# Optimization experiments

Hardware: AMD Instinct MI355X
Metric: run time of the kernel (lower is better)

Reference implementation:

```python
import jax, jax.numpy as jnp
import numpy as np

D_MODEL = 1024
D_INNER = 1024
N_HEADS = 16
HEAD_DIM = D_INNER // N_HEADS  # 64
D_STATE = 16
DT_RANK = 16
CHUNK = 64
PROJ = 2 * D_INNER + 2 * D_STATE * N_HEADS + DT_RANK  # 2576


def setup_inputs() -> dict:
    key = jax.random.key(0)
    ks = jax.random.split(key, 6)
    B, S = 4, 4096
    x = jax.random.normal(ks[0], (B, S, D_MODEL), jnp.float32)
    W_in = jax.random.normal(ks[1], (PROJ, D_MODEL), jnp.float32) * 0.02
    dt_W = jax.random.normal(ks[2], (N_HEADS, DT_RANK), jnp.float32) * 0.1
    dt_b = jax.random.normal(ks[3], (N_HEADS,), jnp.float32) * 0.1
    A_log = jnp.full((N_HEADS,), jnp.log(0.5), jnp.float32)
    D_param = jnp.ones((N_HEADS,), jnp.float32)
    W_out = jax.random.normal(ks[4], (D_MODEL, D_INNER), jnp.float32) * 0.02
    norm_w = jnp.ones((D_INNER,), jnp.float32)
    return dict(x=x, W_in=W_in, dt_W=dt_W, dt_b=dt_b, A_log=A_log,
                D_param=D_param, W_out=W_out, norm_w=norm_w)


def _forward(x, W_in, dt_W, dt_b, A_log, D_param, W_out, norm_w):
    B, S, _ = x.shape
    H, P, N, K = N_HEADS, HEAD_DIM, D_STATE, CHUNK
    proj = x @ W_in.T  # (B,S,PROJ)
    xp = proj[..., :D_INNER]
    z = proj[..., D_INNER:2 * D_INNER]
    o = 2 * D_INNER
    B_ssm = proj[..., o:o + N * H].reshape(B, S, H, N)
    C_ssm = proj[..., o + N * H:o + 2 * N * H].reshape(B, S, H, N)
    dt_low = proj[..., o + 2 * N * H:]
    dt = jax.nn.softplus(dt_low @ dt_W.T + dt_b)  # (B,S,H)
    xp = xp.reshape(B, S, H, P)
    A = -jnp.exp(A_log)  # (H,)

    # --- chunked selective scan (SSD) ---
    nC = S // K  # S chosen divisible by K (original pads otherwise)
    xc = xp.reshape(B, nC, K, H, P)
    dtc = dt.reshape(B, nC, K, H)
    Bc = B_ssm.reshape(B, nC, K, H, N)
    Cc = C_ssm.reshape(B, nC, K, H, N)
    dA = dtc * A  # (B,nC,K,H)
    dAcs = jnp.cumsum(dA, axis=2)
    # intra-chunk quadratic (attention-like) form
    Lm = jnp.exp(dAcs[:, :, :, None, :] - dAcs[:, :, None, :, :])
    causal = jnp.tril(jnp.ones((K, K), jnp.float32))
    Lm = Lm * causal[None, None, :, :, None]
    scores = jnp.einsum('bcihn,bcjhn->bcijh', Cc, Bc) * Lm * dtc[:, :, None, :, :]
    y_intra = jnp.einsum('bcijh,bcjhp->bcihp', scores, xc)
    # per-chunk state contribution
    decay_to_end = jnp.exp(dAcs[:, :, -1:, :] - dAcs)
    wx = (dtc * decay_to_end)[..., None] * xc  # (B,nC,K,H,P)
    chunk_state = jnp.einsum('bckhn,bckhp->bchnp', Bc, wx)  # (B,nC,H,N,P)
    chunk_decay = jnp.exp(dAcs[:, :, -1, :])  # (B,nC,H)

    # cross-chunk recurrence: emit state at chunk START (matches torch loop)
    def step(h, inp):
        d, s = inp
        return d[:, :, None, None] * h + s, h
    h0 = jnp.zeros((B, H, N, P), jnp.float32)
    _, h_states = jax.lax.scan(
        step, h0,
        (jnp.moveaxis(chunk_decay, 1, 0), jnp.moveaxis(chunk_state, 1, 0)))
    h_states = jnp.moveaxis(h_states, 0, 1)  # (B,nC,H,N,P)

    y_cross = jnp.einsum('bcthn,bchnp,bcth->bcthp', Cc, h_states, jnp.exp(dAcs))
    y = (y_intra + y_cross).reshape(B, S, H, P)
    # --- end scan ---

    y = y + xp * D_param[None, None, :, None]
    y = y.reshape(B, S, D_INNER)
    rms = jnp.sqrt(jnp.mean(y * y, axis=-1, keepdims=True) + 1e-6)
    y = y / rms * norm_w
    y = y * jax.nn.silu(z)
    return y @ W_out.T


def reference(x, W_in, dt_W, dt_b, A_log, D_param, W_out, norm_w):
    return _forward(x, W_in, dt_W, dt_b, A_log, D_param, W_out, norm_w)
```

## Files before the change

kernel.cpp:

```cpp
#include <hip/hip_runtime.h>

typedef unsigned short u16;
typedef __attribute__((ext_vector_type(8))) short short8;
typedef __attribute__((ext_vector_type(4))) float f32x4;
typedef __attribute__((ext_vector_type(4))) unsigned short u16x4;
typedef __attribute__((ext_vector_type(8))) unsigned short u16x8;

#define BTOK 16384
#define PROJ_N 2576
#define PROJ_PAD 2688
#define DK 1024
#define NCH 256
#define NH 16
#define HD 64
#define NS 16

__device__ __forceinline__ float b2f(u16 b) {
    union { unsigned int u; float f; } v; v.u = ((unsigned int)b) << 16; return v.f;
}
__device__ __forceinline__ u16 f2b(float f) {
    union { float f; unsigned int u; } v; v.f = f;
    unsigned int r = v.u + 0x7fffu + ((v.u >> 16) & 1u);
    return (u16)(r >> 16);
}
__device__ __forceinline__ void gl_lds16(const u16* g, u16* l) {
    __builtin_amdgcn_global_load_lds((__attribute__((address_space(1))) void*)g,
                                     (__attribute__((address_space(3))) void*)l,
                                     16, 0, 0);
}

__global__ __launch_bounds__(256) void cast_bf16(const float* __restrict__ s,
                                                 u16* __restrict__ d, int n4) {
    int t = blockIdx.x * 256 + threadIdx.x;
    if (t < n4) {
        float4 v = ((const float4*)s)[t];
        u16x4 o; o.x = f2b(v.x); o.y = f2b(v.y); o.z = f2b(v.z); o.w = f2b(v.w);
        ((u16x4*)d)[t] = o;
    }
}

__global__ __launch_bounds__(256) void cast_pad_win(const float* __restrict__ s,
                                                    u16* __restrict__ d) {
    int t = blockIdx.x * 256 + threadIdx.x;
    int i4 = t * 4;
    float4 v = make_float4(0.f, 0.f, 0.f, 0.f);
    if (i4 < PROJ_N * DK) v = ((const float4*)s)[t];
    u16x4 o; o.x = f2b(v.x); o.y = f2b(v.y); o.z = f2b(v.z); o.w = f2b(v.w);
    ((u16x4*)d)[t] = o;
}

template <int OUT_BF16>
__global__ __launch_bounds__(256) void gemm_bt(const u16* __restrict__ A,
                                               const u16* __restrict__ B,
                                               float* __restrict__ Cf,
                                               u16* __restrict__ Cb,
                                               int K, int ldc) {
    __shared__ u16 As[128 * 64];
    __shared__ u16 Bs[128 * 64];
    const int tid = threadIdx.x;
    const int bm = blockIdx.x, bn = blockIdx.y;
    const int wave = tid >> 6, lane = tid & 63;
    const int wm = (wave >> 1) * 64, wn = (wave & 1) * 64;
    const int m_l = lane & 15, quad = lane >> 4;

    f32x4 acc[4][4];
#pragma unroll
    for (int i = 0; i < 4; ++i)
#pragma unroll
        for (int j = 0; j < 4; ++j) acc[i][j] = (f32x4){0.f, 0.f, 0.f, 0.f};

    const u16* Ab = A + (long)bm * 128 * K;
    const u16* Bb = B + (long)bn * 128 * K;

    for (int k0 = 0; k0 < K; k0 += 64) {
#pragma unroll
        for (int it = 0; it < 4; ++it) {
            int li = it * 256 + tid;
            int r = li >> 3;
            int k8 = (li & 7) ^ (r & 7);
            u16* lbase = &As[(it * 256 + wave * 64) * 8];
            gl_lds16(Ab + (long)r * K + k0 + k8 * 8, lbase);
            u16* lbaseB = &Bs[(it * 256 + wave * 64) * 8];
            gl_lds16(Bb + (long)r * K + k0 + k8 * 8, lbaseB);
        }
        __syncthreads();
#pragma unroll
        for (int ks = 0; ks < 2; ++ks) {
            const int k8 = ks * 4 + quad;
            const int slot = k8 ^ (m_l & 7);
            short8 af[4], bf[4];
#pragma unroll
            for (int i = 0; i < 4; ++i) af[i] = *(const short8*)(&As[(wm + i * 16 + m_l) * 64 + slot * 8]);
#pragma unroll
            for (int j = 0; j < 4; ++j) bf[j] = *(const short8*)(&Bs[(wn + j * 16 + m_l) * 64 + slot * 8]);
#pragma unroll
            for (int i = 0; i < 4; ++i)
#pragma unroll
                for (int j = 0; j < 4; ++j)
                    acc[i][j] = __builtin_amdgcn_mfma_f32_16x16x32_bf16(af[i], bf[j], acc[i][j], 0, 0, 0);
        }
        __syncthreads();
    }
#pragma unroll
    for (int i = 0; i < 4; ++i) {
        int row_base = bm * 128 + wm + i * 16 + quad * 4;
#pragma unroll
        for (int j = 0; j < 4; ++j) {
            int col = bn * 128 + wn + j * 16 + m_l;
#pragma unroll
            for (int r = 0; r < 4; ++r) {
                float v = acc[i][j][r];
                long off = (long)(row_base + r) * ldc + col;
                if (OUT_BF16) Cb[off] = f2b(v);
                else          Cf[off] = v;
            }
        }
    }
}

__global__ __launch_bounds__(64) void compute_dt(const u16* __restrict__ proj,
                                                 const float* __restrict__ dt_W,
                                                 const float* __restrict__ dt_b,
                                                 const float* __restrict__ A_log,
                                                 float* __restrict__ dt,
                                                 float* __restrict__ dAcs,
                                                 float* __restrict__ decay) {
    int bc = blockIdx.x;
    int i = threadIdx.x;
    long tok = (long)bc * 64 + i;
    float low[16];
#pragma unroll
    for (int r = 0; r < 16; ++r) low[r] = b2f(proj[tok * PROJ_PAD + 2560 + r]);
#pragma unroll
    for (int h = 0; h < 16; ++h) {
        float a = dt_b[h];
#pragma unroll
        for (int r = 0; r < 16; ++r) a += low[r] * dt_W[h * 16 + r];
        float d = (a > 20.f) ? a : log1pf(__expf(a));
        float dA = -__expf(A_log[h]) * d;
        float cs = dA;
#pragma unroll
        for (int off = 1; off < 64; off <<= 1) {
            float o = __shfl_up(cs, off, 64);
            if (i >= off) cs += o;
        }
        dt[tok * 16 + h] = d;
        dAcs[tok * 16 + h] = cs;
        if (i == 63) decay[bc * 16 + h] = __expf(cs);
    }
}

__global__ __launch_bounds__(256) void ssm_intra(const u16* __restrict__ proj,
                                                 const float* __restrict__ dt,
                                                 const float* __restrict__ dAcs,
                                                 u16* __restrict__ y_acc,
                                                 float* __restrict__ cstate) {
    int bch = blockIdx.x;
    int bc = bch >> 4, h = bch & 15;
    long tok0 = (long)bc * 64;
    __shared__ float Cs[64][16], Bm[64][16];
    __shared__ u16 Sh[64][64], Sl[64][64];
    __shared__ u16 Xt[64][64];
    __shared__ u16 Wh[64][64], Wl[64][64];
    __shared__ u16 Bt[16][64];
    __shared__ float dts[64], dAs[64], wk[64];
    const int tid = threadIdx.x;
    const int wave = tid >> 6, lane = tid & 63;
    const int m_l = lane & 15, quad = lane >> 4;

    if (tid < 64) {
        dts[tid] = dt[(tok0 + tid) * 16 + h];
        dAs[tid] = dAcs[(tok0 + tid) * 16 + h];
    }
    if (tid < 64) wk[tid] = dts[tid] * __expf(dAs[63] - dAs[tid]);
#pragma unroll
    for (int it = 0; it < 4; ++it) {
        int li = it * 256 + tid;
        int i = li >> 4, n = li & 15;
        u16 cb = proj[(tok0 + i) * PROJ_PAD + 2304 + h * 16 + n];
        u16 bb = proj[(tok0 + i) * PROJ_PAD + 2048 + h * 16 + n];
        Cs[i][n] = b2f(cb);
        Bm[i][n] = b2f(bb);
        Bt[n][i] = bb;
    }
    __syncthreads();
#pragma unroll
    for (int it = 0; it < 2; ++it) {
        int li = it * 256 + tid;
        int j = li & 63, p0 = (li >> 6) * 8;
        u16x8 xv = *(const u16x8*)&proj[(tok0 + j) * PROJ_PAD + h * 64 + p0];
        float w = wk[j];
#pragma unroll
        for (int t = 0; t < 8; ++t) {
            u16 xb = xv[t];
            Xt[p0 + t][j] = xb;
            float v = w * b2f(xb);
            u16 hi = f2b(v);
            Wh[p0 + t][j] = hi;
            Wl[p0 + t][j] = f2b(v - b2f(hi));
        }
    }
    {
        int j = tid & 63, i0 = tid >> 6;
#pragma unroll
        for (int g = 0; g < 16; ++g) {
            int i = i0 + g * 4;
            float v = 0.f;
            if (j <= i) {
                float d = 0.f;
                const f32x4* cp = (const f32x4*)Cs[i];
                const f32x4* bp = (const f32x4*)Bm[j];
#pragma unroll
                for (int n4 = 0; n4 < 4; ++n4) {
                    f32x4 c = cp[n4], b = bp[n4];
                    d += c.x * b.x + c.y * b.y + c.z * b.z + c.w * b.w;
                }
                v = d * __expf(dAs[i] - dAs[j]) * dts[j];
            }
            u16 hi = f2b(v);
            Sh[i][j] = hi;
            Sl[i][j] = f2b(v - b2f(hi));
        }
    }
    __syncthreads();
    {
        f32x4 yv[4];
#pragma unroll
        for (int jt = 0; jt < 4; ++jt) yv[jt] = (f32x4){0.f, 0.f, 0.f, 0.f};
#pragma unroll
        for (int ks = 0; ks < 2; ++ks) {
            int kc = ks * 32 + quad * 8;
            short8 ah = *(const short8*)&Sh[wave * 16 + m_l][kc];
            short8 al = *(const short8*)&Sl[wave * 16 + m_l][kc];
#pragma unroll
            for (int jt = 0; jt < 4; ++jt) {
                short8 bx = *(const short8*)&Xt[jt * 16 + m_l][kc];
                yv[jt] = __builtin_amdgcn_mfma_f32_16x16x32_bf16(ah, bx, yv[jt], 0, 0, 0);
                yv[jt] = __builtin_amdgcn_mfma_f32_16x16x32_bf16(al, bx, yv[jt], 0, 0, 0);
            }
        }
#pragma unroll
        for (int jt = 0; jt < 4; ++jt)
#pragma unroll
            for (int r = 0; r < 4; ++r) {
                int i = wave * 16 + quad * 4 + r;
                int p = jt * 16 + m_l;
                y_acc[(tok0 + i) * 1024 + h * 64 + p] = f2b(yv[jt][r]);
            }
    }
    {
        f32x4 cacc = (f32x4){0.f, 0.f, 0.f, 0.f};
#pragma unroll
        for (int ks = 0; ks < 2; ++ks) {
            int kc = ks * 32 + quad * 8;
            short8 a = *(const short8*)&Bt[m_l][kc];
            short8 bh = *(const short8*)&Wh[wave * 16 + m_l][kc];
            short8 bl = *(const short8*)&Wl[wave * 16 + m_l][kc];
            cacc = __builtin_amdgcn_mfma_f32_16x16x32_bf16(a, bh, cacc, 0, 0, 0);
            cacc = __builtin_amdgcn_mfma_f32_16x16x32_bf16(a, bl, cacc, 0, 0, 0);
        }
#pragma unroll
        for (int r = 0; r < 4; ++r) {
            int n = quad * 4 + r;
            int p = wave * 16 + m_l;
            cstate[(long)bch * 1024 + n * 64 + p] = cacc[r];
        }
    }
}

__global__ __launch_bounds__(256) void scan_chunks(const float* __restrict__ cs,
                                                   const float* __restrict__ decay,
                                                   float* __restrict__ hs) {
    int t = blockIdx.x * 256 + threadIdx.x;
    int p = t & 63, n = (t >> 6) & 15, h = (t >> 10) & 15, b = t >> 14;
    float state = 0.f;
    for (int c = 0; c < 64; ++c) {
        long idx = (((long)((b * 64 + c) * 16 + h)) * 16 + n) * 64 + p;
        hs[idx] = state;
        state = decay[(b * 64 + c) * 16 + h] * state + cs[idx];
    }
}

__global__ __launch_bounds__(256) void ssm_cross(const u16* __restrict__ proj,
                                                 const float* __restrict__ dAcs,
                                                 const float* __restrict__ hs,
                                                 const u16* __restrict__ y_acc,
                                                 const float* __restrict__ D_param,
                                                 u16* __restrict__ y_pre) {
    int bch = blockIdx.x;
    int bc = bch >> 4, h = bch & 15;
    long tok0 = (long)bc * 64;
    __shared__ float hss[16][64], Cs[64][16], dAs[64];
    int tid = threadIdx.x;
#pragma unroll
    for (int it = 0; it < 4; ++it) {
        int li = it * 256 + tid;
        hss[li >> 6][li & 63] = hs[(long)bch * 1024 + li];
        int i = li >> 4, n = li & 15;
        Cs[i][n] = b2f(proj[(tok0 + i) * PROJ_PAD + 2304 + h * 16 + n]);
    }
    if (tid < 64) dAs[tid] = dAcs[(tok0 + tid) * 16 + h];
    __syncthreads();
    float Dh = D_param[h];
    int pi = (tid & 15) * 4;
    int ib = tid >> 4;
#pragma unroll
    for (int g = 0; g < 4; ++g) {
        int i = ib + 16 * g;
        f32x4 cr = (f32x4){0.f, 0.f, 0.f, 0.f};
#pragma unroll
        for (int n = 0; n < 16; ++n) {
            float c = Cs[i][n];
            cr += c * *(const f32x4*)&hss[n][pi];
        }
        float e = __expf(dAs[i]);
        long off = (tok0 + i) * 1024 + h * 64 + pi;
        u16x4 ya = *(const u16x4*)&y_acc[off];
        u16x4 xv = *(const u16x4*)&proj[(tok0 + i) * PROJ_PAD + h * 64 + pi];
        u16x4 o;
        o.x = f2b(b2f(ya.x) + e * cr.x + b2f(xv.x) * Dh);
        o.y = f2b(b2f(ya.y) + e * cr.y + b2f(xv.y) * Dh);
        o.z = f2b(b2f(ya.z) + e * cr.z + b2f(xv.z) * Dh);
        o.w = f2b(b2f(ya.w) + e * cr.w + b2f(xv.w) * Dh);
        *(u16x4*)&y_pre[off] = o;
    }
}

__global__ __launch_bounds__(256) void norm_gate(const u16* __restrict__ proj,
                                                 const float* __restrict__ norm_w,
                                                 u16* __restrict__ y) {
    long tok = blockIdx.x;
    int tid = threadIdx.x;
    int c0 = tid * 4;
    u16x4 yv = *(const u16x4*)&y[tok * 1024 + c0];
    float v0 = b2f(yv.x), v1 = b2f(yv.y), v2 = b2f(yv.z), v3 = b2f(yv.w);
    float ss = v0 * v0 + v1 * v1 + v2 * v2 + v3 * v3;
    int lane = tid & 63, w = tid >> 6;
#pragma unroll
    for (int d = 32; d > 0; d >>= 1) ss += __shfl_down(ss, d, 64);
    __shared__ float red[4];
    if (lane == 0) red[w] = ss;
    __syncthreads();
    float tot = red[0] + red[1] + red[2] + red[3];
    float inv = rsqrtf(tot * (1.f / 1024.f) + 1e-6f);
    float4 nw = *(const float4*)&norm_w[c0];
    u16x4 zv = *(const u16x4*)&proj[tok * PROJ_PAD + 1024 + c0];
    float z0 = b2f(zv.x), z1 = b2f(zv.y), z2 = b2f(zv.z), z3 = b2f(zv.w);
    u16x4 o;
    o.x = f2b(v0 * inv * nw.x * (z0 / (1.f + __expf(-z0))));
    o.y = f2b(v1 * inv * nw.y * (z1 / (1.f + __expf(-z1))));
    o.z = f2b(v2 * inv * nw.z * (z2 / (1.f + __expf(-z2))));
    o.w = f2b(v3 * inv * nw.w * (z3 / (1.f + __expf(-z3))));
    *(u16x4*)&y[tok * 1024 + c0] = o;
}

extern "C" void kernel_launch(void* const* d_in, const int* in_sizes, int n_in,
                              void* d_out, int out_size, void* d_ws, size_t ws_size,
                              hipStream_t stream) {
    const float* x      = (const float*)d_in[0];
    const float* W_in   = (const float*)d_in[1];
    const float* dt_W   = (const float*)d_in[2];
    const float* dt_b   = (const float*)d_in[3];
    const float* A_log  = (const float*)d_in[4];
    const float* D_par  = (const float*)d_in[5];
    const float* W_out  = (const float*)d_in[6];
    const float* norm_w = (const float*)d_in[7];
    float* out = (float*)d_out;

    char* ws = (char*)d_ws;
    size_t off = 0;
    auto alloc = [&](size_t b) { void* p = ws + off; off += (b + 255) & ~(size_t)255; return p; };
    u16*   x_bf    = (u16*)alloc((size_t)BTOK * DK * 2);
    u16*   win_bf  = (u16*)alloc((size_t)PROJ_PAD * DK * 2);
    u16*   wout_bf = (u16*)alloc((size_t)DK * DK * 2);
    u16*   proj    = (u16*)alloc((size_t)BTOK * PROJ_PAD * 2);
    float* dt      = (float*)alloc((size_t)BTOK * NH * 4);
    float* dAcs    = (float*)alloc((size_t)BTOK * NH * 4);
    float* decay   = (float*)alloc((size_t)NCH * NH * 4);
    float* cstate  = (float*)alloc((size_t)NCH * NH * NS * HD * 4);
    float* hstates = (float*)alloc((size_t)NCH * NH * NS * HD * 4);
    u16*   y_pre   = (u16*)alloc((size_t)BTOK * DK * 2);
    u16*   y_acc   = x_bf;

    cast_bf16<<<BTOK * DK / 4 / 256, 256, 0, stream>>>(x, x_bf, BTOK * DK / 4);
    cast_bf16<<<DK * DK / 4 / 256, 256, 0, stream>>>(W_out, wout_bf, DK * DK / 4);
    cast_pad_win<<<PROJ_PAD * DK / 4 / 256, 256, 0, stream>>>(W_in, win_bf);

    gemm_bt<1><<<dim3(128, 21), 256, 0, stream>>>(x_bf, win_bf, nullptr, proj, DK, PROJ_PAD);

    compute_dt<<<NCH, 64, 0, stream>>>(proj, dt_W, dt_b, A_log, dt, dAcs, decay);
    ssm_intra<<<NCH * NH, 256, 0, stream>>>(proj, dt, dAcs, y_acc, cstate);
    scan_chunks<<<256, 256, 0, stream>>>(cstate, decay, hstates);
    ssm_cross<<<NCH * NH, 256, 0, stream>>>(proj, dAcs, hstates, y_acc, D_par, y_pre);
    norm_gate<<<BTOK, 256, 0, stream>>>(proj, norm_w, y_pre);

    gemm_bt<0><<<dim3(128, 8), 256, 0, stream>>>(y_pre, wout_bf, out, nullptr, DK, DK);
}
```

Measured before the change: 412.5 us.

## Fuse dt computation into ssm_intra and pad shared arrays against bank conflicts

```diff
diff --git a/kernel.cpp b/kernel.cpp
--- a/kernel.cpp
+++ b/kernel.cpp
@@ -118,61 +118,51 @@
     }
 }
 
-__global__ __launch_bounds__(64) void compute_dt(const u16* __restrict__ proj,
+__global__ __launch_bounds__(256) void ssm_intra(const u16* __restrict__ proj,
                                                  const float* __restrict__ dt_W,
                                                  const float* __restrict__ dt_b,
                                                  const float* __restrict__ A_log,
-                                                 float* __restrict__ dt,
                                                  float* __restrict__ dAcs,
-                                                 float* __restrict__ decay) {
-    int bc = blockIdx.x;
-    int i = threadIdx.x;
-    long tok = (long)bc * 64 + i;
-    float low[16];
-#pragma unroll
-    for (int r = 0; r < 16; ++r) low[r] = b2f(proj[tok * PROJ_PAD + 2560 + r]);
-#pragma unroll
-    for (int h = 0; h < 16; ++h) {
-        float a = dt_b[h];
-#pragma unroll
-        for (int r = 0; r < 16; ++r) a += low[r] * dt_W[h * 16 + r];
-        float d = (a > 20.f) ? a : log1pf(__expf(a));
-        float dA = -__expf(A_log[h]) * d;
-        float cs = dA;
-#pragma unroll
-        for (int off = 1; off < 64; off <<= 1) {
-            float o = __shfl_up(cs, off, 64);
-            if (i >= off) cs += o;
-        }
-        dt[tok * 16 + h] = d;
-        dAcs[tok * 16 + h] = cs;
-        if (i == 63) decay[bc * 16 + h] = __expf(cs);
-    }
-}
-
-__global__ __launch_bounds__(256) void ssm_intra(const u16* __restrict__ proj,
-                                                 const float* __restrict__ dt,
-                                                 const float* __restrict__ dAcs,
+                                                 float* __restrict__ decay,
                                                  u16* __restrict__ y_acc,
                                                  float* __restrict__ cstate) {
     int bch = blockIdx.x;
     int bc = bch >> 4, h = bch & 15;
     long tok0 = (long)bc * 64;
-    __shared__ float Cs[64][16], Bm[64][16];
-    __shared__ u16 Sh[64][64], Sl[64][64];
-    __shared__ u16 Xt[64][64];
-    __shared__ u16 Wh[64][64], Wl[64][64];
-    __shared__ u16 Bt[16][64];
+    __shared__ float Cs[64][20], Bm[64][20];
+    __shared__ u16 Sh[64][72], Sl[64][72];
+    __shared__ u16 Xt[64][72];
+    __shared__ u16 Wh[64][72], Wl[64][72];
+    __shared__ u16 Bt[16][72];
     __shared__ float dts[64], dAs[64], wk[64];
     const int tid = threadIdx.x;
     const int wave = tid >> 6, lane = tid & 63;
     const int m_l = lane & 15, quad = lane >> 4;
 
     if (tid < 64) {
-        dts[tid] = dt[(tok0 + tid) * 16 + h];
-        dAs[tid] = dAcs[(tok0 + tid) * 16 + h];
-    }
-    if (tid < 64) wk[tid] = dts[tid] * __expf(dAs[63] - dAs[tid]);
+        long tok = tok0 + tid;
+        u16x8 lo0 = *(const u16x8*)&proj[tok * PROJ_PAD + 2560];
+        u16x8 lo1 = *(const u16x8*)&proj[tok * PROJ_PAD + 2568];
+        float a = dt_b[h];
+#pragma unroll
+        for (int r = 0; r < 8; ++r) a += b2f(lo0[r]) * dt_W[h * 16 + r];
+#pragma unroll
+        for (int r = 0; r < 8; ++r) a += b2f(lo1[r]) * dt_W[h * 16 + 8 + r];
+        float d = (a > 20.f) ? a : log1pf(__expf(a));
+        float dA = -__expf(A_log[h]) * d;
+        float cs = dA;
+#pragma unroll
+        for (int off = 1; off < 64; off <<= 1) {
+            float o = __shfl_up(cs, off, 64);
+            if (tid >= off) cs += o;
+        }
+        float cs63 = __shfl(cs, 63, 64);
+        dts[tid] = d;
+        dAs[tid] = cs;
+        wk[tid] = d * __expf(cs63 - cs);
+        dAcs[tok * 16 + h] = cs;
+        if (tid == 63) decay[bc * 16 + h] = __expf(cs);
+    }
 #pragma unroll
     for (int it = 0; it < 4; ++it) {
         int li = it * 256 + tid;
@@ -374,7 +364,6 @@
     u16*   win_bf  = (u16*)alloc((size_t)PROJ_PAD * DK * 2);
     u16*   wout_bf = (u16*)alloc((size_t)DK * DK * 2);
     u16*   proj    = (u16*)alloc((size_t)BTOK * PROJ_PAD * 2);
-    float* dt      = (float*)alloc((size_t)BTOK * NH * 4);
     float* dAcs    = (float*)alloc((size_t)BTOK * NH * 4);
     float* decay   = (float*)alloc((size_t)NCH * NH * 4);
     float* cstate  = (float*)alloc((size_t)NCH * NH * NS * HD * 4);
@@ -388,8 +377,7 @@
 
     gemm_bt<1><<<dim3(128, 21), 256, 0, stream>>>(x_bf, win_bf, nullptr, proj, DK, PROJ_PAD);
 
-    compute_dt<<<NCH, 64, 0, stream>>>(proj, dt_W, dt_b, A_log, dt, dAcs, decay);
-    ssm_intra<<<NCH * NH, 256, 0, stream>>>(proj, dt, dAcs, y_acc, cstate);
+    ssm_intra<<<NCH * NH, 256, 0, stream>>>(proj, dt_W, dt_b, A_log, dAcs, decay, y_acc, cstate);
     scan_chunks<<<256, 256, 0, stream>>>(cstate, decay, hstates);
     ssm_cross<<<NCH * NH, 256, 0, stream>>>(proj, dAcs, hstates, y_acc, D_par, y_pre);
     norm_gate<<<BTOK, 256, 0, stream>>>(proj, norm_w, y_pre);
```

After: 397.9 us. -3.6%, faster.
